# Performance work log

Hardware: AMD Instinct MI355X
Metric: run time of the kernel (lower is better)

The kernel has to match this reference:

```python
import jax, jax.numpy as jnp
import numpy as np

EPS = 1e-5

def conv1x1(x, w, b):
    # x: [B,C,H,W], w: [O,C], b: [O]
    return jnp.einsum('bchw,oc->bohw', x, w) + b[None, :, None, None]

def batchnorm(x, gamma, beta):
    # training-mode BN: biased batch statistics over (N,H,W)
    mean = jnp.mean(x, axis=(0, 2, 3), keepdims=True)
    var = jnp.var(x, axis=(0, 2, 3), keepdims=True)
    inv = jax.lax.rsqrt(var + EPS)
    return (x - mean) * inv * gamma[None, :, None, None] + beta[None, :, None, None]

def setup_inputs() -> dict:
    key = jax.random.key(0)
    ks = jax.random.split(key, 20)
    B, H, W = 32, 480, 640
    d = {
        'x1': jax.random.normal(ks[0], (B, 3, H, W), dtype=jnp.float32),
        'w1': jax.random.normal(ks[1], (3, 3), dtype=jnp.float32) * 0.3,
        'b1': jax.random.normal(ks[2], (3,), dtype=jnp.float32) * 0.1,
        'g2': jnp.ones((3,), dtype=jnp.float32),
        'be2': jnp.zeros((3,), dtype=jnp.float32),
        'w3': jax.random.normal(ks[3], (8, 3), dtype=jnp.float32) * 0.3,
        'b3': jax.random.normal(ks[4], (8,), dtype=jnp.float32) * 0.1,
        'w4': jax.random.normal(ks[5], (8, 8), dtype=jnp.float32) * 0.2,
        'b4': jax.random.normal(ks[6], (8,), dtype=jnp.float32) * 0.1,
        'g5': jnp.ones((8,), dtype=jnp.float32),
        'be5': jnp.zeros((8,), dtype=jnp.float32),
        'w6': jax.random.normal(ks[7], (8, 8), dtype=jnp.float32) * 0.2,
        'b6': jax.random.normal(ks[8], (8,), dtype=jnp.float32) * 0.1,
        'w7': jax.random.normal(ks[9], (8, 8), dtype=jnp.float32) * 0.2,
        'b7': jax.random.normal(ks[10], (8,), dtype=jnp.float32) * 0.1,
        'w8': jax.random.normal(ks[11], (8, 8), dtype=jnp.float32) * 0.2,
        'b8': jax.random.normal(ks[12], (8,), dtype=jnp.float32) * 0.1,
    }
    return d

def reference(x1, w1, b1, g2, be2, w3, b3, w4, b4, g5, be5, w6, b6, w7, b7, w8, b8):
    v1 = conv1x1(x1, w1, b1)        # [B,3,H,W]
    v2 = batchnorm(v1, g2, be2)     # [B,3,H,W]
    v3 = conv1x1(v2, w3, b3)        # [B,8,H,W]
    v4 = conv1x1(v3, w4, b4)
    v5 = batchnorm(v4, g5, be5)
    v6 = conv1x1(v5, w6, b6)
    v7 = conv1x1(v6, w7, b7)
    v8 = conv1x1(v7, w8, b8)
    return v8
```

## Files before the change

kernel.cpp:

```cpp
#include <hip/hip_runtime.h>
#include <math.h>

#define HWD   (480*640)
#define HW4   (HWD/4)
#define BATCH 32
#define NPIXD ((double)BATCH*(double)HWD)
#define NPIX4 (BATCH*HW4)
#define RBLK  1024
#define BPI   32
#define ISTRIDE (BPI*256)
#define BN_EPS 1e-5

typedef float f32x4 __attribute__((ext_vector_type(4)));

__global__ __launch_bounds__(256) void k_reduce(const float* __restrict__ x,
                                                double* __restrict__ partials) {
    const int b   = blockIdx.x >> 5;
    const int blk = blockIdx.x & 31;
    const float4* xb = (const float4*)x + (long long)b*(3*HW4);

    float s0=0.f,s1=0.f,s2=0.f,s00=0.f,s01=0.f,s02=0.f,s11=0.f,s12=0.f,s22=0.f;
    for (int s = blk*256 + threadIdx.x; s < HW4; s += ISTRIDE) {
        const float4 a = xb[s];
        const float4 c = xb[s + HW4];
        const float4 e = xb[s + 2*HW4];
        float X0,X1,X2;
        X0=a.x; X1=c.x; X2=e.x;
        s0+=X0; s1+=X1; s2+=X2;
        s00=fmaf(X0,X0,s00); s01=fmaf(X0,X1,s01); s02=fmaf(X0,X2,s02);
        s11=fmaf(X1,X1,s11); s12=fmaf(X1,X2,s12); s22=fmaf(X2,X2,s22);
        X0=a.y; X1=c.y; X2=e.y;
        s0+=X0; s1+=X1; s2+=X2;
        s00=fmaf(X0,X0,s00); s01=fmaf(X0,X1,s01); s02=fmaf(X0,X2,s02);
        s11=fmaf(X1,X1,s11); s12=fmaf(X1,X2,s12); s22=fmaf(X2,X2,s22);
        X0=a.z; X1=c.z; X2=e.z;
        s0+=X0; s1+=X1; s2+=X2;
        s00=fmaf(X0,X0,s00); s01=fmaf(X0,X1,s01); s02=fmaf(X0,X2,s02);
        s11=fmaf(X1,X1,s11); s12=fmaf(X1,X2,s12); s22=fmaf(X2,X2,s22);
        X0=a.w; X1=c.w; X2=e.w;
        s0+=X0; s1+=X1; s2+=X2;
        s00=fmaf(X0,X0,s00); s01=fmaf(X0,X1,s01); s02=fmaf(X0,X2,s02);
        s11=fmaf(X1,X1,s11); s12=fmaf(X1,X2,s12); s22=fmaf(X2,X2,s22);
    }
    double v[9] = {(double)s0,(double)s1,(double)s2,(double)s00,(double)s01,
                   (double)s02,(double)s11,(double)s12,(double)s22};
    #pragma unroll
    for (int off = 32; off > 0; off >>= 1) {
        #pragma unroll
        for (int q = 0; q < 9; ++q) v[q] += __shfl_down(v[q], off, 64);
    }
    __shared__ double lds[4][9];
    const int lane = threadIdx.x & 63;
    const int wid  = threadIdx.x >> 6;
    if (lane == 0) {
        #pragma unroll
        for (int q = 0; q < 9; ++q) lds[wid][q] = v[q];
    }
    __syncthreads();
    if (threadIdx.x < 9) {
        partials[(long long)blockIdx.x*9 + threadIdx.x] =
            lds[0][threadIdx.x] + lds[1][threadIdx.x] + lds[2][threadIdx.x] + lds[3][threadIdx.x];
    }
}

__device__ void affine8(const float* __restrict__ w, const float* __restrict__ bias,
                        double A[8][3], double cc[8]) {
    double T[8][3], tc[8];
    for (int o = 0; o < 8; ++o) {
        double t0=0,t1=0,t2=0,tb=0;
        for (int c = 0; c < 8; ++c) {
            const double wv = (double)w[o*8+c];
            t0 += wv*A[c][0]; t1 += wv*A[c][1]; t2 += wv*A[c][2]; tb += wv*cc[c];
        }
        T[o][0]=t0; T[o][1]=t1; T[o][2]=t2; tc[o]=tb + (double)bias[o];
    }
    for (int o = 0; o < 8; ++o) { A[o][0]=T[o][0]; A[o][1]=T[o][1]; A[o][2]=T[o][2]; cc[o]=tc[o]; }
}

__device__ void bn8(int rows, const double m[3], const double C[3][3],
                    const float* __restrict__ g, const float* __restrict__ be,
                    double A[8][3], double cc[8]) {
    for (int o = 0; o < rows; ++o) {
        const double mu = A[o][0]*m[0] + A[o][1]*m[1] + A[o][2]*m[2] + cc[o];
        double var = 0;
        for (int i = 0; i < 3; ++i)
            for (int j = 0; j < 3; ++j)
                var += A[o][i]*A[o][j]*C[i][j];
        const double inv = 1.0 / sqrt(var + BN_EPS);
        const double sc  = inv * (double)g[o];
        A[o][0]*=sc; A[o][1]*=sc; A[o][2]*=sc;
        cc[o] = (cc[o]-mu)*sc + (double)be[o];
    }
}

__global__ __launch_bounds__(1024) void k_params(const double* __restrict__ partials,
        const float* __restrict__ w1, const float* __restrict__ b1,
        const float* __restrict__ g2, const float* __restrict__ be2,
        const float* __restrict__ w3, const float* __restrict__ b3,
        const float* __restrict__ w4, const float* __restrict__ b4,
        const float* __restrict__ g5, const float* __restrict__ be5,
        const float* __restrict__ w6, const float* __restrict__ b6,
        const float* __restrict__ w7, const float* __restrict__ b7,
        const float* __restrict__ w8, const float* __restrict__ b8,
        float* __restrict__ Md) {
    const int tid = threadIdx.x;
    double v[9];
    #pragma unroll
    for (int q = 0; q < 9; ++q) v[q] = partials[(long long)tid*9 + q];
    #pragma unroll
    for (int off = 32; off > 0; off >>= 1) {
        #pragma unroll
        for (int q = 0; q < 9; ++q) v[q] += __shfl_down(v[q], off, 64);
    }
    __shared__ double lds[16][9];
    const int lane = tid & 63;
    const int wid  = tid >> 6;
    if (lane == 0) {
        #pragma unroll
        for (int q = 0; q < 9; ++q) lds[wid][q] = v[q];
    }
    __syncthreads();
    __shared__ double red[9];
    if (tid < 9) {
        double acc = 0.0;
        #pragma unroll
        for (int w = 0; w < 16; ++w) acc += lds[w][tid];
        red[tid] = acc;
    }
    __syncthreads();
    if (tid != 0) return;

    const double N = NPIXD;
    double m[3];
    for (int i = 0; i < 3; ++i) m[i] = red[i] / N;
    double S[3][3];
    S[0][0]=red[3]; S[0][1]=red[4]; S[0][2]=red[5];
    S[1][1]=red[6]; S[1][2]=red[7]; S[2][2]=red[8];
    S[1][0]=S[0][1]; S[2][0]=S[0][2]; S[2][1]=S[1][2];
    double C[3][3];
    for (int i = 0; i < 3; ++i)
        for (int j = 0; j < 3; ++j)
            C[i][j] = S[i][j]/N - m[i]*m[j];

    double A[8][3], cc[8];
    for (int o = 0; o < 3; ++o) {
        A[o][0]=(double)w1[o*3+0]; A[o][1]=(double)w1[o*3+1]; A[o][2]=(double)w1[o*3+2];
        cc[o]=(double)b1[o];
    }
    bn8(3, m, C, g2, be2, A, cc);
    {
        double T[8][3], tc[8];
        for (int o = 0; o < 8; ++o) {
            double t0=0,t1=0,t2=0,tb=0;
            for (int c = 0; c < 3; ++c) {
                const double wv = (double)w3[o*3+c];
                t0 += wv*A[c][0]; t1 += wv*A[c][1]; t2 += wv*A[c][2]; tb += wv*cc[c];
            }
            T[o][0]=t0; T[o][1]=t1; T[o][2]=t2; tc[o]=tb + (double)b3[o];
        }
        for (int o = 0; o < 8; ++o) { A[o][0]=T[o][0]; A[o][1]=T[o][1]; A[o][2]=T[o][2]; cc[o]=tc[o]; }
    }
    affine8(w4, b4, A, cc);
    bn8(8, m, C, g5, be5, A, cc);
    affine8(w6, b6, A, cc);
    affine8(w7, b7, A, cc);
    affine8(w8, b8, A, cc);
    for (int o = 0; o < 8; ++o) {
        Md[o*4+0] = (float)A[o][0];
        Md[o*4+1] = (float)A[o][1];
        Md[o*4+2] = (float)A[o][2];
        Md[o*4+3] = (float)cc[o];
    }
}

__global__ __launch_bounds__(256) void k_apply(const float* __restrict__ x,
                                               const float* __restrict__ Md,
                                               float* __restrict__ out) {
    const int t = blockIdx.x*blockDim.x + threadIdx.x;
    const int b = t / HW4;
    const int s = t - b*HW4;
    const float4* xb = (const float4*)x + (long long)b*(3*HW4) + s;
    const float4 x0 = xb[0];
    const float4 x1 = xb[HW4];
    const float4 x2 = xb[2*HW4];
    f32x4* ob = (f32x4*)out + (long long)b*(8*HW4) + s;
    const float4* M4 = (const float4*)Md;
    #pragma unroll
    for (int o = 0; o < 8; ++o) {
        const float4 mr = M4[o];
        f32x4 r;
        r.x = fmaf(mr.x, x0.x, fmaf(mr.y, x1.x, fmaf(mr.z, x2.x, mr.w)));
        r.y = fmaf(mr.x, x0.y, fmaf(mr.y, x1.y, fmaf(mr.z, x2.y, mr.w)));
        r.z = fmaf(mr.x, x0.z, fmaf(mr.y, x1.z, fmaf(mr.z, x2.z, mr.w)));
        r.w = fmaf(mr.x, x0.w, fmaf(mr.y, x1.w, fmaf(mr.z, x2.w, mr.w)));
        __builtin_nontemporal_store(r, ob + (long long)o*HW4);
    }
}

extern "C" void kernel_launch(void* const* d_in, const int* in_sizes, int n_in,
                              void* d_out, int out_size, void* d_ws, size_t ws_size,
                              hipStream_t stream) {
    const float* x  = (const float*)d_in[0];
    const float* w1 = (const float*)d_in[1];
    const float* b1 = (const float*)d_in[2];
    const float* g2 = (const float*)d_in[3];
    const float* be2= (const float*)d_in[4];
    const float* w3 = (const float*)d_in[5];
    const float* b3 = (const float*)d_in[6];
    const float* w4 = (const float*)d_in[7];
    const float* b4 = (const float*)d_in[8];
    const float* g5 = (const float*)d_in[9];
    const float* be5= (const float*)d_in[10];
    const float* w6 = (const float*)d_in[11];
    const float* b6 = (const float*)d_in[12];
    const float* w7 = (const float*)d_in[13];
    const float* b7 = (const float*)d_in[14];
    const float* w8 = (const float*)d_in[15];
    const float* b8 = (const float*)d_in[16];

    double* partials = (double*)d_ws;
    float*  Md       = (float*)((char*)d_ws + (size_t)RBLK*9*sizeof(double));
    float*  out      = (float*)d_out;

    k_reduce<<<RBLK, 256, 0, stream>>>(x, partials);
    k_params<<<1, 1024, 0, stream>>>(partials,
        w1,b1,g2,be2,w3,b3,w4,b4,g5,be5,w6,b6,w7,b7,w8,b8, Md);
    k_apply<<<NPIX4/256, 256, 0, stream>>>(x, Md, out);
}
```

Before: 105.6 us.

## Fuse parameter computation into apply kernel with grid-stride loop

Removes the single-block parameter kernel and has every apply block redundantly reduce the 1024 partial statistics and fold the BN/conv chain into an 8x4 affine matrix in shared memory. The apply stage becomes a grid-stride loop over 1024 blocks instead of one thread per float4. This eliminates a kernel launch and a serial dependency, at the cost of redundant per-block reductions and a serial double-precision preamble in each block.

```diff
diff --git a/kernel.cpp b/kernel.cpp
--- a/kernel.cpp
+++ b/kernel.cpp
@@ -93,7 +93,8 @@
     }
 }
 
-__global__ __launch_bounds__(1024) void k_params(const double* __restrict__ partials,
+__global__ __launch_bounds__(256) void k_apply2(const float* __restrict__ x,
+        const double* __restrict__ partials,
         const float* __restrict__ w1, const float* __restrict__ b1,
         const float* __restrict__ g2, const float* __restrict__ be2,
         const float* __restrict__ w3, const float* __restrict__ b3,
@@ -102,98 +103,98 @@
         const float* __restrict__ w6, const float* __restrict__ b6,
         const float* __restrict__ w7, const float* __restrict__ b7,
         const float* __restrict__ w8, const float* __restrict__ b8,
-        float* __restrict__ Md) {
-    const int tid = threadIdx.x;
-    double v[9];
+        float* __restrict__ out) {
+    __shared__ float4 MdS[8];
+    {
+        const int tid = threadIdx.x;
+        double v[9] = {0,0,0,0,0,0,0,0,0};
+        #pragma unroll
+        for (int r = 0; r < 4; ++r) {
+            const double* row = partials + (size_t)(r*256 + tid)*9;
+            #pragma unroll
+            for (int q = 0; q < 9; ++q) v[q] += row[q];
+        }
+        #pragma unroll
+        for (int off = 32; off > 0; off >>= 1) {
+            #pragma unroll
+            for (int q = 0; q < 9; ++q) v[q] += __shfl_down(v[q], off, 64);
+        }
+        __shared__ double wsum[4][9];
+        __shared__ double red[9];
+        const int lane = tid & 63;
+        const int wid  = tid >> 6;
+        if (lane == 0) {
+            #pragma unroll
+            for (int q = 0; q < 9; ++q) wsum[wid][q] = v[q];
+        }
+        __syncthreads();
+        if (tid < 9) red[tid] = wsum[0][tid] + wsum[1][tid] + wsum[2][tid] + wsum[3][tid];
+        __syncthreads();
+
+        if (tid == 0) {
+            const double N = NPIXD;
+            double m[3];
+            for (int i = 0; i < 3; ++i) m[i] = red[i] / N;
+            double S[3][3];
+            S[0][0]=red[3]; S[0][1]=red[4]; S[0][2]=red[5];
+            S[1][1]=red[6]; S[1][2]=red[7]; S[2][2]=red[8];
+            S[1][0]=S[0][1]; S[2][0]=S[0][2]; S[2][1]=S[1][2];
+            double C[3][3];
+            for (int i = 0; i < 3; ++i)
+                for (int j = 0; j < 3; ++j)
+                    C[i][j] = S[i][j]/N - m[i]*m[j];
+
+            double A[8][3], cc[8];
+            for (int o = 0; o < 3; ++o) {
+                A[o][0]=(double)w1[o*3+0]; A[o][1]=(double)w1[o*3+1]; A[o][2]=(double)w1[o*3+2];
+                cc[o]=(double)b1[o];
+            }
+            bn8(3, m, C, g2, be2, A, cc);
+            {
+                double T[8][3], tc[8];
+                for (int o = 0; o < 8; ++o) {
+                    double t0=0,t1=0,t2=0,tb=0;
+                    for (int c = 0; c < 3; ++c) {
+                        const double wv = (double)w3[o*3+c];
+                        t0 += wv*A[c][0]; t1 += wv*A[c][1]; t2 += wv*A[c][2]; tb += wv*cc[c];
+                    }
+                    T[o][0]=t0; T[o][1]=t1; T[o][2]=t2; tc[o]=tb + (double)b3[o];
+                }
+                for (int o = 0; o < 8; ++o) { A[o][0]=T[o][0]; A[o][1]=T[o][1]; A[o][2]=T[o][2]; cc[o]=tc[o]; }
+            }
+            affine8(w4, b4, A, cc);
+            bn8(8, m, C, g5, be5, A, cc);
+            affine8(w6, b6, A, cc);
+            affine8(w7, b7, A, cc);
+            affine8(w8, b8, A, cc);
+            for (int o = 0; o < 8; ++o)
+                MdS[o] = make_float4((float)A[o][0], (float)A[o][1], (float)A[o][2], (float)cc[o]);
+        }
+        __syncthreads();
+    }
+
+    const int b   = blockIdx.x >> 5;
+    const int blk = blockIdx.x & 31;
+    const float4* xb = (const float4*)x + (long long)b*(3*HW4);
+    f32x4* ob = (f32x4*)out + (long long)b*(8*HW4);
+    float4 M[8];
     #pragma unroll
-    for (int q = 0; q < 9; ++q) v[q] = partials[(long long)tid*9 + q];
-    #pragma unroll
-    for (int off = 32; off > 0; off >>= 1) {
-        #pragma unroll
-        for (int q = 0; q < 9; ++q) v[q] += __shfl_down(v[q], off, 64);
-    }
-    __shared__ double lds[16][9];
-    const int lane = tid & 63;
-    const int wid  = tid >> 6;
-    if (lane == 0) {
-        #pragma unroll
-        for (int q = 0; q < 9; ++q) lds[wid][q] = v[q];
-    }
-    __syncthreads();
-    __shared__ double red[9];
-    if (tid < 9) {
-        double acc = 0.0;
-        #pragma unroll
-        for (int w = 0; w < 16; ++w) acc += lds[w][tid];
-        red[tid] = acc;
-    }
-    __syncthreads();
-    if (tid != 0) return;
-
-    const double N = NPIXD;
-    double m[3];
-    for (int i = 0; i < 3; ++i) m[i] = red[i] / N;
-    double S[3][3];
-    S[0][0]=red[3]; S[0][1]=red[4]; S[0][2]=red[5];
-    S[1][1]=red[6]; S[1][2]=red[7]; S[2][2]=red[8];
-    S[1][0]=S[0][1]; S[2][0]=S[0][2]; S[2][1]=S[1][2];
-    double C[3][3];
-    for (int i = 0; i < 3; ++i)
-        for (int j = 0; j < 3; ++j)
-            C[i][j] = S[i][j]/N - m[i]*m[j];
-
-    double A[8][3], cc[8];
-    for (int o = 0; o < 3; ++o) {
-        A[o][0]=(double)w1[o*3+0]; A[o][1]=(double)w1[o*3+1]; A[o][2]=(double)w1[o*3+2];
-        cc[o]=(double)b1[o];
-    }
-    bn8(3, m, C, g2, be2, A, cc);
-    {
-        double T[8][3], tc[8];
+    for (int o = 0; o < 8; ++o) M[o] = MdS[o];
+
+    for (int s = blk*256 + threadIdx.x; s < HW4; s += ISTRIDE) {
+        const float4 x0 = xb[s];
+        const float4 x1 = xb[s + HW4];
+        const float4 x2 = xb[s + 2*HW4];
+        #pragma unroll
         for (int o = 0; o < 8; ++o) {
-            double t0=0,t1=0,t2=0,tb=0;
-            for (int c = 0; c < 3; ++c) {
-                const double wv = (double)w3[o*3+c];
-                t0 += wv*A[c][0]; t1 += wv*A[c][1]; t2 += wv*A[c][2]; tb += wv*cc[c];
-            }
-            T[o][0]=t0; T[o][1]=t1; T[o][2]=t2; tc[o]=tb + (double)b3[o];
-        }
-        for (int o = 0; o < 8; ++o) { A[o][0]=T[o][0]; A[o][1]=T[o][1]; A[o][2]=T[o][2]; cc[o]=tc[o]; }
-    }
-    affine8(w4, b4, A, cc);
-    bn8(8, m, C, g5, be5, A, cc);
-    affine8(w6, b6, A, cc);
-    affine8(w7, b7, A, cc);
-    affine8(w8, b8, A, cc);
-    for (int o = 0; o < 8; ++o) {
-        Md[o*4+0] = (float)A[o][0];
-        Md[o*4+1] = (float)A[o][1];
-        Md[o*4+2] = (float)A[o][2];
-        Md[o*4+3] = (float)cc[o];
-    }
-}
-
-__global__ __launch_bounds__(256) void k_apply(const float* __restrict__ x,
-                                               const float* __restrict__ Md,
-                                               float* __restrict__ out) {
-    const int t = blockIdx.x*blockDim.x + threadIdx.x;
-    const int b = t / HW4;
-    const int s = t - b*HW4;
-    const float4* xb = (const float4*)x + (long long)b*(3*HW4) + s;
-    const float4 x0 = xb[0];
-    const float4 x1 = xb[HW4];
-    const float4 x2 = xb[2*HW4];
-    f32x4* ob = (f32x4*)out + (long long)b*(8*HW4) + s;
-    const float4* M4 = (const float4*)Md;
-    #pragma unroll
-    for (int o = 0; o < 8; ++o) {
-        const float4 mr = M4[o];
-        f32x4 r;
-        r.x = fmaf(mr.x, x0.x, fmaf(mr.y, x1.x, fmaf(mr.z, x2.x, mr.w)));
-        r.y = fmaf(mr.x, x0.y, fmaf(mr.y, x1.y, fmaf(mr.z, x2.y, mr.w)));
-        r.z = fmaf(mr.x, x0.z, fmaf(mr.y, x1.z, fmaf(mr.z, x2.z, mr.w)));
-        r.w = fmaf(mr.x, x0.w, fmaf(mr.y, x1.w, fmaf(mr.z, x2.w, mr.w)));
-        __builtin_nontemporal_store(r, ob + (long long)o*HW4);
+            const float4 mr = M[o];
+            f32x4 r;
+            r.x = fmaf(mr.x, x0.x, fmaf(mr.y, x1.x, fmaf(mr.z, x2.x, mr.w)));
+            r.y = fmaf(mr.x, x0.y, fmaf(mr.y, x1.y, fmaf(mr.z, x2.y, mr.w)));
+            r.z = fmaf(mr.x, x0.z, fmaf(mr.y, x1.z, fmaf(mr.z, x2.z, mr.w)));
+            r.w = fmaf(mr.x, x0.w, fmaf(mr.y, x1.w, fmaf(mr.z, x2.w, mr.w)));
+            __builtin_nontemporal_store(r, ob + (long long)o*HW4 + s);
+        }
     }
 }
 
@@ -219,11 +220,9 @@
     const float* b8 = (const float*)d_in[16];
 
     double* partials = (double*)d_ws;
-    float*  Md       = (float*)((char*)d_ws + (size_t)RBLK*9*sizeof(double));
     float*  out      = (float*)d_out;
 
     k_reduce<<<RBLK, 256, 0, stream>>>(x, partials);
-    k_params<<<1, 1024, 0, stream>>>(partials,
-        w1,b1,g2,be2,w3,b3,w4,b4,g5,be5,w6,b6,w7,b7,w8,b8, Md);
-    k_apply<<<NPIX4/256, 256, 0, stream>>>(x, Md, out);
-}
+    k_apply2<<<RBLK, 256, 0, stream>>>(x, partials,
+        w1,b1,g2,be2,w3,b3,w4,b4,g5,be5,w6,b6,w7,b7,w8,b8, out);
+}
```

New measurement: 103.0 us. 1.02x faster.
